# Performance work log

Hardware: AMD Instinct MI355X
Metric: run time of the kernel (lower is better)

The kernel has to match this reference:

```python
import jax, jax.numpy as jnp
import numpy as np

NEG_SLOPE = 0.2  # PyG GATConv default LeakyReLU slope
BN_EPS = 1e-5


def gat_layer(x, src, dst, W, a_src, a_dst, num_nodes):
    """PyG-style GATConv (no dropout, eval mode). Returns [N, H, C]."""
    H, C = a_src.shape
    h = (x @ W).reshape(-1, H, C)                       # [N,H,C]
    s_src = jnp.einsum('nhc,hc->nh', h, a_src)          # [N,H]
    s_dst = jnp.einsum('nhc,hc->nh', h, a_dst)          # [N,H]
    e = jax.nn.leaky_relu(s_src[src] + s_dst[dst], NEG_SLOPE)  # [E,H]
    # segment softmax over incoming edges of each dst node
    e_max = jax.ops.segment_max(e, dst, num_segments=num_nodes)  # [N,H]
    e_exp = jnp.exp(e - e_max[dst])
    denom = jax.ops.segment_sum(e_exp, dst, num_segments=num_nodes)
    alpha = e_exp / (denom[dst] + 1e-16)                # [E,H]
    msg = h[src] * alpha[:, :, None]                    # [E,H,C] (dominant intermediate)
    return jax.ops.segment_sum(msg, dst, num_segments=num_nodes)  # [N,H,C]


def setup_inputs() -> dict:
    key = jax.random.key(0)
    ks = jax.random.split(key, 12)
    N, Din, Hdim, Heads, Dout = 50000, 128, 128, 8, 128
    E = 150000
    inp = {}
    inp['x'] = jax.random.normal(ks[0], (N, Din), dtype=jnp.float32)
    inp['edge_index'] = jax.random.randint(ks[1], (2, E), 0, N, dtype=jnp.int64)
    sc1 = 1.0 / np.sqrt(Din)
    inp['W1'] = jax.random.uniform(ks[2], (Din, Heads * Hdim), minval=-sc1, maxval=sc1, dtype=jnp.float32)
    inp['a_src1'] = jax.random.normal(ks[3], (Heads, Hdim), dtype=jnp.float32) * 0.1
    inp['a_dst1'] = jax.random.normal(ks[4], (Heads, Hdim), dtype=jnp.float32) * 0.1
    inp['b1'] = jnp.zeros((Heads * Hdim,), dtype=jnp.float32)
    inp['gamma'] = jnp.ones((Heads * Hdim,), dtype=jnp.float32)
    inp['beta'] = jnp.zeros((Heads * Hdim,), dtype=jnp.float32)
    sc2 = 1.0 / np.sqrt(Heads * Hdim)
    inp['W2'] = jax.random.uniform(ks[5], (Heads * Hdim, Dout), minval=-sc2, maxval=sc2, dtype=jnp.float32)
    inp['a_src2'] = jax.random.normal(ks[6], (1, Dout), dtype=jnp.float32) * 0.1
    inp['a_dst2'] = jax.random.normal(ks[7], (1, Dout), dtype=jnp.float32) * 0.1
    inp['b2'] = jnp.zeros((Dout,), dtype=jnp.float32)
    return inp


def reference(x, W1, a_src1, a_dst1, b1, gamma, beta, W2, a_src2, a_dst2, b2, edge_index):
    N = x.shape[0]
    src, dst = edge_index[0], edge_index[1]
    # GAT layer 1: heads=8, concat=True
    h1 = gat_layer(x, src, dst, W1, a_src1, a_dst1, N)   # [N,8,128]
    h1 = h1.reshape(N, -1) + b1                          # [N,1024]
    # BatchNorm1d (training-mode batch stats, biased variance as in torch)
    mu = jnp.mean(h1, axis=0)
    var = jnp.var(h1, axis=0)
    h1 = gamma * (h1 - mu) * jax.lax.rsqrt(var + BN_EPS) + beta
    h1 = jax.nn.elu(h1)
    # GAT layer 2: heads=1, concat=False (mean == squeeze for 1 head)
    h2 = gat_layer(h1, src, dst, W2, a_src2, a_dst2, N)  # [N,1,128]
    return h2[:, 0, :] + b2
```

## Files before the change

kernel.cpp:

```cpp
#include <hip/hip_runtime.h>
#include <hip/hip_bf16.h>
#include <math.h>

#define NEG_SLOPE 0.2f
#define BN_EPS 1e-5f

typedef short bf16x8 __attribute__((ext_vector_type(8)));
typedef float f32x4 __attribute__((ext_vector_type(4)));

__device__ __forceinline__ float bf2f(unsigned short u) {
  union { unsigned int i; float f; } v;
  v.i = ((unsigned int)u) << 16;
  return v.f;
}
__device__ __forceinline__ unsigned short f2bf(float f) {
  union { unsigned int i; float f; } v;
  v.f = f;
  unsigned int i = v.i;
  unsigned int r = (i + 0x7fffu + ((i >> 16) & 1u)) >> 16;
  return (unsigned short)r;
}

__global__ __launch_bounds__(256) void detect_kernel(
    const unsigned int* __restrict__ xw, const unsigned int* __restrict__ eiw,
    int E, int* __restrict__ flags) {
  __shared__ int cnt[2];
  if (threadIdx.x < 2) cnt[threadIdx.x] = 0;
  __syncthreads();
  int t = threadIdx.x;
  int inrange = 0;
  for (int i = t; i < 2048; i += 256) {
    unsigned int e = (xw[i] >> 7) & 0xFFu;
    inrange += (e >= 100u && e <= 135u) ? 1 : 0;
  }
  atomicAdd(&cnt[0], inrange);
  int M = min(1024, E / 2);
  int zeros = 0;
  for (int i = t; i < M; i += 256) zeros += (eiw[2 * i + 1] == 0u) ? 1 : 0;
  atomicAdd(&cnt[1], zeros);
  __syncthreads();
  if (t == 0) {
    flags[0] = (cnt[0] > 1536) ? 1 : 0;
    flags[1] = (cnt[1] > M / 2) ? 1 : 0;
  }
}

__global__ __launch_bounds__(256) void canon_x(
    const void* __restrict__ src, unsigned short* __restrict__ dst, int n_real,
    int n_total, const int* __restrict__ flags) {
  int i = blockIdx.x * 256 + threadIdx.x;
  if (i >= n_total) return;
  unsigned short v = 0;
  if (i < n_real)
    v = flags[0] ? ((const unsigned short*)src)[i]
                 : f2bf(((const float*)src)[i]);
  dst[i] = v;
}

__global__ __launch_bounds__(256) void canon_w_t(
    const void* __restrict__ src, unsigned short* __restrict__ dst, int Kdim,
    int Ndim, const int* __restrict__ flags) {
  int i = blockIdx.x * 256 + threadIdx.x;
  if (i >= Kdim * Ndim) return;
  int k = i / Ndim, n = i - k * Ndim;
  unsigned short v = flags[0] ? ((const unsigned short*)src)[i]
                              : f2bf(((const float*)src)[i]);
  dst[(size_t)n * Kdim + k] = v;
}

__global__ __launch_bounds__(1024) void canon_params(
    const void* s0, const void* s1, const void* s2, const void* s3,
    const void* s4, const void* s5, const void* s6, const void* s7,
    unsigned short* d0, unsigned short* d1, unsigned short* d2,
    unsigned short* d3, unsigned short* d4, unsigned short* d5,
    unsigned short* d6, unsigned short* d7, const int* __restrict__ flags) {
  int b = blockIdx.x, t = threadIdx.x;
  const void* s;
  unsigned short* d;
  int n;
  switch (b) {
    case 0: s = s0; d = d0; n = 1024; break;
    case 1: s = s1; d = d1; n = 1024; break;
    case 2: s = s2; d = d2; n = 1024; break;
    case 3: s = s3; d = d3; n = 1024; break;
    case 4: s = s4; d = d4; n = 1024; break;
    case 5: s = s5; d = d5; n = 128; break;
    case 6: s = s6; d = d6; n = 128; break;
    default: s = s7; d = d7; n = 128; break;
  }
  if (t < n)
    d[t] = flags[0] ? ((const unsigned short*)s)[t]
                    : f2bf(((const float*)s)[t]);
}

__global__ __launch_bounds__(256) void canon_idx(
    const int* __restrict__ ei, int* __restrict__ eis, int* __restrict__ eid,
    int E, const int* __restrict__ flags) {
  int e = blockIdx.x * 256 + threadIdx.x;
  if (e >= E) return;
  if (flags[1]) {
    eis[e] = ei[2 * (size_t)e];
    eid[e] = ei[2 * (size_t)E + 2 * (size_t)e];
  } else {
    eis[e] = ei[e];
    eid[e] = ei[E + e];
  }
}

template <bool TRANSFORM_A, bool OUT_BF16>
__global__ __launch_bounds__(256) void gemm_mfma(
    const unsigned short* __restrict__ A, const unsigned short* __restrict__ Bt,
    void* __restrict__ Cv, int M, int N, int K,
    const float* __restrict__ scale, const float* __restrict__ shift) {
  constexpr int BK = 32;
  constexpr int LDA = BK + 8;
  __shared__ unsigned short As[128 * LDA];
  __shared__ unsigned short Bs[128 * LDA];

  const int m0 = blockIdx.y * 128;
  const int n0 = blockIdx.x * 128;
  const int tid = threadIdx.x;
  const int wid = tid >> 6;
  const int lane = tid & 63;
  const int q = lane >> 4;
  const int r = lane & 15;
  const int wm = (wid >> 1) * 64;
  const int wn = (wid & 1) * 64;

  f32x4 acc[4][4] = {};

  const int row0 = (tid * 8) >> 5, col0 = (tid * 8) & 31;
  const int row1 = row0 + 64;

  bf16x8 ra[2], rb[2];
  ra[0] = *(const bf16x8*)(A + (size_t)(m0 + row0) * K + col0);
  ra[1] = *(const bf16x8*)(A + (size_t)(m0 + row1) * K + col0);
  rb[0] = *(const bf16x8*)(Bt + (size_t)(n0 + row0) * K + col0);
  rb[1] = *(const bf16x8*)(Bt + (size_t)(n0 + row1) * K + col0);

  for (int k0 = 0; k0 < K; k0 += BK) {
#pragma unroll
    for (int rd = 0; rd < 2; ++rd) {
      int row = rd ? row1 : row0;
      bf16x8 v = ra[rd];
      if (TRANSFORM_A) {
        float scv[8], shv[8];
        *(float4*)&scv[0] = *(const float4*)(scale + k0 + col0);
        *(float4*)&scv[4] = *(const float4*)(scale + k0 + col0 + 4);
        *(float4*)&shv[0] = *(const float4*)(shift + k0 + col0);
        *(float4*)&shv[4] = *(const float4*)(shift + k0 + col0 + 4);
        union { bf16x8 v; unsigned short u[8]; } p;
        p.v = v;
#pragma unroll
        for (int j = 0; j < 8; ++j) {
          float f = bf2f(p.u[j]) * scv[j] + shv[j];
          f = f > 0.f ? f : (__expf(f) - 1.0f);
          p.u[j] = f2bf(f);
        }
        v = p.v;
      }
      *(bf16x8*)(&As[row * LDA + col0]) = v;
      *(bf16x8*)(&Bs[row * LDA + col0]) = rb[rd];
    }
    __syncthreads();

    int k1 = k0 + BK;
    if (k1 < K) {
      ra[0] = *(const bf16x8*)(A + (size_t)(m0 + row0) * K + k1 + col0);
      ra[1] = *(const bf16x8*)(A + (size_t)(m0 + row1) * K + k1 + col0);
      rb[0] = *(const bf16x8*)(Bt + (size_t)(n0 + row0) * K + k1 + col0);
      rb[1] = *(const bf16x8*)(Bt + (size_t)(n0 + row1) * K + k1 + col0);
    }

    bf16x8 af[4], bfv[4];
#pragma unroll
    for (int mi = 0; mi < 4; ++mi)
      af[mi] = *(const bf16x8*)(&As[(wm + mi * 16 + r) * LDA + q * 8]);
#pragma unroll
    for (int ni = 0; ni < 4; ++ni)
      bfv[ni] = *(const bf16x8*)(&Bs[(wn + ni * 16 + r) * LDA + q * 8]);
#pragma unroll
    for (int mi = 0; mi < 4; ++mi)
#pragma unroll
      for (int ni = 0; ni < 4; ++ni)
        acc[mi][ni] = __builtin_amdgcn_mfma_f32_16x16x32_bf16(
            af[mi], bfv[ni], acc[mi][ni], 0, 0, 0);
    __syncthreads();
  }

#pragma unroll
  for (int mi = 0; mi < 4; ++mi) {
#pragma unroll
    for (int ni = 0; ni < 4; ++ni) {
#pragma unroll
      for (int i = 0; i < 4; ++i) {
        int row = m0 + wm + mi * 16 + q * 4 + i;
        int col = n0 + wn + ni * 16 + r;
        if (OUT_BF16)
          ((unsigned short*)Cv)[(size_t)row * N + col] = f2bf(acc[mi][ni][i]);
        else
          ((float*)Cv)[(size_t)row * N + col] = acc[mi][ni][i];
      }
    }
  }
}

__global__ __launch_bounds__(256) void count_dst(const int* __restrict__ eid,
                                                 int E, int* __restrict__ cnt) {
  int e = blockIdx.x * 256 + threadIdx.x;
  if (e < E) atomicAdd(&cnt[eid[e]], 1);
}

__global__ __launch_bounds__(256) void scan_p1(const int* __restrict__ cnt,
                                               int* __restrict__ bsum, int N) {
  __shared__ int sd[256];
  int b = blockIdx.x, t = threadIdx.x;
  int base = b * 2048;
  int s = 0;
  for (int i = t; i < 2048; i += 256) {
    int idx = base + i;
    if (idx < N) s += cnt[idx];
  }
  sd[t] = s;
  __syncthreads();
  for (int o = 128; o > 0; o >>= 1) {
    if (t < o) sd[t] += sd[t + o];
    __syncthreads();
  }
  if (t == 0) bsum[b] = sd[0];
}

__global__ __launch_bounds__(256) void scan_p2(int* __restrict__ bsum, int nb) {
  __shared__ int sd[256];
  int t = threadIdx.x;
  int own = (t < nb) ? bsum[t] : 0;
  sd[t] = own;
  __syncthreads();
  for (int o = 1; o < 256; o <<= 1) {
    int v = (t >= o) ? sd[t - o] : 0;
    __syncthreads();
    sd[t] += v;
    __syncthreads();
  }
  if (t < nb) bsum[t] = sd[t] - own;
}

__global__ __launch_bounds__(256) void scan_p3(
    const int* __restrict__ cnt, const int* __restrict__ bsum,
    int* __restrict__ offsets, int* __restrict__ cursor, int N) {
  __shared__ int sd[256];
  int b = blockIdx.x, t = threadIdx.x;
  int base = b * 2048 + t * 8;
  int c[8];
  int ts = 0;
#pragma unroll
  for (int j = 0; j < 8; ++j) {
    int idx = base + j;
    c[j] = (idx < N) ? cnt[idx] : 0;
    ts += c[j];
  }
  sd[t] = ts;
  __syncthreads();
  for (int o = 1; o < 256; o <<= 1) {
    int v = (t >= o) ? sd[t - o] : 0;
    __syncthreads();
    sd[t] += v;
    __syncthreads();
  }
  int run = bsum[b] + sd[t] - ts;
#pragma unroll
  for (int j = 0; j < 8; ++j) {
    int idx = base + j;
    if (idx < N) {
      offsets[idx] = run;
      cursor[idx] = run;
      run += c[j];
    }
  }
  if (b == gridDim.x - 1 && t == 255) offsets[N] = bsum[b] + sd[255];
}

__global__ __launch_bounds__(256) void scatter_src(
    const int* __restrict__ eis, const int* __restrict__ eid, int E,
    int* __restrict__ cursor, int* __restrict__ srcs, int* __restrict__ dsts) {
  int e = blockIdx.x * 256 + threadIdx.x;
  if (e >= E) return;
  int d = eid[e];
  int pos = atomicAdd(&cursor[d], 1);
  srcs[pos] = eis[e];
  dsts[pos] = d;
}

__global__ __launch_bounds__(256) void scores1_v2(
    const unsigned short* __restrict__ h1, const unsigned short* __restrict__ a_src,
    const unsigned short* __restrict__ a_dst, float* __restrict__ s_src,
    float* __restrict__ s_dst, int N) {
  int n = blockIdx.x * 4 + (threadIdx.x >> 6);
  int lane = threadIdx.x & 63;
  if (n >= N) return;
  const unsigned short* hp = h1 + (size_t)n * 1024 + lane * 16;
  union { bf16x8 v; unsigned short u[8]; } h0, h1v, s0, s1, d0, d1;
  h0.v = *(const bf16x8*)hp;
  h1v.v = *(const bf16x8*)(hp + 8);
  s0.v = *(const bf16x8*)(a_src + lane * 16);
  s1.v = *(const bf16x8*)(a_src + lane * 16 + 8);
  d0.v = *(const bf16x8*)(a_dst + lane * 16);
  d1.v = *(const bf16x8*)(a_dst + lane * 16 + 8);
  float vs = 0.f, vd = 0.f;
#pragma unroll
  for (int j = 0; j < 8; ++j) {
    float a = bf2f(h0.u[j]), b = bf2f(h1v.u[j]);
    vs += a * bf2f(s0.u[j]) + b * bf2f(s1.u[j]);
    vd += a * bf2f(d0.u[j]) + b * bf2f(d1.u[j]);
  }
  vs += __shfl_xor(vs, 1, 64); vd += __shfl_xor(vd, 1, 64);
  vs += __shfl_xor(vs, 2, 64); vd += __shfl_xor(vd, 2, 64);
  vs += __shfl_xor(vs, 4, 64); vd += __shfl_xor(vd, 4, 64);
  if ((lane & 7) == 0) {
    int h = lane >> 3;
    s_src[n * 8 + h] = vs;
    s_dst[n * 8 + h] = vd;
  }
}

__global__ __launch_bounds__(256) void scores2_f32(
    const float* __restrict__ h2, const unsigned short* __restrict__ a_src,
    const unsigned short* __restrict__ a_dst, float* __restrict__ s_src,
    float* __restrict__ s_dst, int N) {
  int w = blockIdx.x * 4 + (threadIdx.x >> 6);
  int lane = threadIdx.x & 63;
  if (w >= N) return;
  float2 hv = *(const float2*)(h2 + (size_t)w * 128 + lane * 2);
  unsigned int av = *(const unsigned int*)(a_src + lane * 2);
  unsigned int dv = *(const unsigned int*)(a_dst + lane * 2);
  float vs = hv.x * bf2f(av & 0xffff) + hv.y * bf2f(av >> 16);
  float vd = hv.x * bf2f(dv & 0xffff) + hv.y * bf2f(dv >> 16);
#pragma unroll
  for (int off = 32; off > 0; off >>= 1) {
    vs += __shfl_down(vs, off, 64);
    vd += __shfl_down(vd, off, 64);
  }
  if (lane == 0) {
    s_src[w] = vs;
    s_dst[w] = vd;
  }
}

__global__ __launch_bounds__(256) void edge_w1(
    const int* __restrict__ srcs, const int* __restrict__ dsts,
    const float* __restrict__ ssrc, const float* __restrict__ sdst,
    float* __restrict__ ew, int E8) {
  int t = blockIdx.x * 256 + threadIdx.x;
  if (t >= E8) return;
  int p = t >> 3, h = t & 7;
  float v = ssrc[srcs[p] * 8 + h] + sdst[dsts[p] * 8 + h];
  v = v > 0.f ? v : NEG_SLOPE * v;
  ew[t] = __expf(v);
}

__global__ __launch_bounds__(256) void edge_w2(
    const int* __restrict__ srcs, const int* __restrict__ dsts,
    const float* __restrict__ ssrc, const float* __restrict__ sdst,
    float* __restrict__ ew2, int E) {
  int p = blockIdx.x * 256 + threadIdx.x;
  if (p >= E) return;
  float v = ssrc[srcs[p]] + sdst[dsts[p]];
  v = v > 0.f ? v : NEG_SLOPE * v;
  ew2[p] = __expf(v);
}

__global__ __launch_bounds__(256) void agg1_csr(
    const int* __restrict__ offsets, const int* __restrict__ srcs,
    const unsigned short* __restrict__ h1, const float* __restrict__ ew,
    const unsigned short* __restrict__ b1, unsigned short* __restrict__ h1n) {
  int n = blockIdx.x;
  int j = threadIdx.x;
  int c = j * 4;
  int h = c >> 7;
  int beg = offsets[n], end = offsets[n + 1];
  float a0 = 0.f, a1 = 0.f, a2 = 0.f, a3 = 0.f, wsum = 0.f;
  for (int p = beg; p < end; ++p) {
    int s = srcs[p];
    float w = ew[p * 8 + h];
    wsum += w;
    ushort4 u = *(const ushort4*)(h1 + (size_t)s * 1024 + c);
    a0 = fmaf(bf2f(u.x), w, a0);
    a1 = fmaf(bf2f(u.y), w, a1);
    a2 = fmaf(bf2f(u.z), w, a2);
    a3 = fmaf(bf2f(u.w), w, a3);
  }
  float inv = 1.0f / (wsum + 1e-16f);
  ushort4 bb = *(const ushort4*)(b1 + c);
  ushort4 o;
  o.x = f2bf(a0 * inv + bf2f(bb.x));
  o.y = f2bf(a1 * inv + bf2f(bb.y));
  o.z = f2bf(a2 * inv + bf2f(bb.z));
  o.w = f2bf(a3 * inv + bf2f(bb.w));
  *(ushort4*)(h1n + (size_t)n * 1024 + c) = o;
}

__global__ __launch_bounds__(256) void bn_stats_part(
    const unsigned short* __restrict__ h1n, float* __restrict__ part, int N,
    int rowsPerBlock) {
  int b = blockIdx.x;
  int r0 = b * rowsPerBlock;
  int r1 = min(r0 + rowsPerBlock, N);
  int c = threadIdx.x * 4;
  float s0 = 0, s1 = 0, s2 = 0, s3 = 0;
  float q0 = 0, q1 = 0, q2 = 0, q3 = 0;
  int r = r0;
  for (; r + 4 <= r1; r += 4) {
    ushort4 u0 = *(const ushort4*)(h1n + (size_t)(r + 0) * 1024 + c);
    ushort4 u1 = *(const ushort4*)(h1n + (size_t)(r + 1) * 1024 + c);
    ushort4 u2 = *(const ushort4*)(h1n + (size_t)(r + 2) * 1024 + c);
    ushort4 u3 = *(const ushort4*)(h1n + (size_t)(r + 3) * 1024 + c);
    float v;
    v = bf2f(u0.x); s0 += v; q0 += v * v;
    v = bf2f(u0.y); s1 += v; q1 += v * v;
    v = bf2f(u0.z); s2 += v; q2 += v * v;
    v = bf2f(u0.w); s3 += v; q3 += v * v;
    v = bf2f(u1.x); s0 += v; q0 += v * v;
    v = bf2f(u1.y); s1 += v; q1 += v * v;
    v = bf2f(u1.z); s2 += v; q2 += v * v;
    v = bf2f(u1.w); s3 += v; q3 += v * v;
    v = bf2f(u2.x); s0 += v; q0 += v * v;
    v = bf2f(u2.y); s1 += v; q1 += v * v;
    v = bf2f(u2.z); s2 += v; q2 += v * v;
    v = bf2f(u2.w); s3 += v; q3 += v * v;
    v = bf2f(u3.x); s0 += v; q0 += v * v;
    v = bf2f(u3.y); s1 += v; q1 += v * v;
    v = bf2f(u3.z); s2 += v; q2 += v * v;
    v = bf2f(u3.w); s3 += v; q3 += v * v;
  }
  for (; r < r1; ++r) {
    ushort4 u = *(const ushort4*)(h1n + (size_t)r * 1024 + c);
    float v;
    v = bf2f(u.x); s0 += v; q0 += v * v;
    v = bf2f(u.y); s1 += v; q1 += v * v;
    v = bf2f(u.z); s2 += v; q2 += v * v;
    v = bf2f(u.w); s3 += v; q3 += v * v;
  }
  float* pb = part + (size_t)b * 2048;
  pb[c + 0] = s0; pb[c + 1] = s1; pb[c + 2] = s2; pb[c + 3] = s3;
  pb[1024 + c + 0] = q0; pb[1024 + c + 1] = q1;
  pb[1024 + c + 2] = q2; pb[1024 + c + 3] = q3;
}

__global__ __launch_bounds__(256) void bn_reduce_finalize(
    const float* __restrict__ part, int nparts,
    const unsigned short* __restrict__ gamma,
    const unsigned short* __restrict__ beta, float* __restrict__ scale,
    float* __restrict__ shift, int N) {
  int c = blockIdx.x * 4 + (threadIdx.x >> 6);
  int lane = threadIdx.x & 63;
  float s = 0.f, q = 0.f;
  for (int b = lane; b < nparts; b += 64) {
    s += part[(size_t)b * 2048 + c];
    q += part[(size_t)b * 2048 + 1024 + c];
  }
#pragma unroll
  for (int o = 32; o > 0; o >>= 1) {
    s += __shfl_xor(s, o, 64);
    q += __shfl_xor(q, o, 64);
  }
  if (lane == 0) {
    float inv_n = 1.0f / (float)N;
    float mu = s * inv_n;
    float var = q * inv_n - mu * mu;
    float sc = bf2f(gamma[c]) * rsqrtf(var + BN_EPS);
    scale[c] = sc;
    shift[c] = bf2f(beta[c]) - mu * sc;
  }
}

__global__ __launch_bounds__(64) void agg2_csr(
    const int* __restrict__ offsets, const int* __restrict__ srcs,
    const float* __restrict__ h2, const float* __restrict__ ew2,
    const unsigned short* __restrict__ b2, void* __restrict__ out,
    const int* __restrict__ flags) {
  int n = blockIdx.x;
  int lane = threadIdx.x;
  int c = lane * 2;
  int beg = offsets[n], end = offsets[n + 1];
  float a0 = 0.f, a1 = 0.f, wsum = 0.f;
  for (int p = beg; p < end; ++p) {
    int s = srcs[p];
    float w = ew2[p];
    wsum += w;
    float2 hv = *(const float2*)(h2 + (size_t)s * 128 + c);
    a0 = fmaf(hv.x, w, a0);
    a1 = fmaf(hv.y, w, a1);
  }
  float inv = 1.0f / (wsum + 1e-16f);
  unsigned int bb = *(const unsigned int*)(b2 + c);
  float r0 = a0 * inv + bf2f(bb & 0xffff);
  float r1 = a1 * inv + bf2f(bb >> 16);
  if (flags[0]) {
    unsigned int o = (unsigned int)f2bf(r0) | ((unsigned int)f2bf(r1) << 16);
    *(unsigned int*)((unsigned short*)out + (size_t)n * 128 + c) = o;
  } else {
    *(float2*)((float*)out + (size_t)n * 128 + c) = make_float2(r0, r1);
  }
}

extern "C" void kernel_launch(void* const* d_in, const int* in_sizes, int n_in,
                              void* d_out, int out_size, void* d_ws,
                              size_t ws_size, hipStream_t stream) {
  const void* x      = d_in[0];
  const int*  ei     = (const int*)d_in[1];
  const void* W1     = d_in[2];
  const void* a_src1 = d_in[3];
  const void* a_dst1 = d_in[4];
  const void* b1     = d_in[5];
  const void* gamma  = d_in[6];
  const void* beta   = d_in[7];
  const void* W2     = d_in[8];
  const void* a_src2 = d_in[9];
  const void* a_dst2 = d_in[10];
  const void* b2     = d_in[11];

  const int N = in_sizes[0] / 128;
  const int E = in_sizes[1] / 2;
  const int MP = ((N + 127) / 128) * 128;
  const int NB = (N + 2047) / 2048;
  const int NSTAT = 256;
  const int RPB = (N + NSTAT - 1) / NSTAT;

  char* ws = (char*)d_ws;
  size_t off = 0;
  unsigned short* h1  = (unsigned short*)(ws + off); off += (size_t)MP * 1024 * 2;
  char* h1n_base = ws + off;
  unsigned short* h1n = (unsigned short*)h1n_base;   off += (size_t)MP * 1024 * 2;
  float* ssrc1 = (float*)(ws + off); off += (size_t)N * 8 * 4;
  float* sdst1 = (float*)(ws + off); off += (size_t)N * 8 * 4;
  int* offsets = (int*)(ws + off); off += ((size_t)(N + 1) * 4 + 63) & ~63ull;
  int* srcs    = (int*)(ws + off); off += (size_t)E * 4;
  int* dsts    = (int*)(ws + off); off += (size_t)E * 4;
  float* ew    = (float*)(ws + off); off += (size_t)E * 8 * 4;
  float* part  = (float*)(ws + off); off += (size_t)NSTAT * 2048 * 4;
  unsigned short* W1t = (unsigned short*)(ws + off); off += 131072 * 2;
  unsigned short* W2t = (unsigned short*)(ws + off); off += 131072 * 2;
  unsigned short* as1c = (unsigned short*)(ws + off); off += 1024 * 2;
  unsigned short* ad1c = (unsigned short*)(ws + off); off += 1024 * 2;
  unsigned short* b1c  = (unsigned short*)(ws + off); off += 1024 * 2;
  unsigned short* gmc  = (unsigned short*)(ws + off); off += 1024 * 2;
  unsigned short* btc  = (unsigned short*)(ws + off); off += 1024 * 2;
  unsigned short* as2c = (unsigned short*)(ws + off); off += 128 * 2;
  unsigned short* ad2c = (unsigned short*)(ws + off); off += 128 * 2;
  unsigned short* b2c  = (unsigned short*)(ws + off); off += 128 * 2;
  float* scale = (float*)(ws + off); off += 1024 * 4;
  float* shift = (float*)(ws + off); off += 1024 * 4;
  int* bsum    = (int*)(ws + off); off += 256 * 4;
  int* flags   = (int*)(ws + off); off += 64;
  unsigned short* x_bf = (unsigned short*)h1n_base;
  int* eis    = (int*)(h1n_base + (16u << 20));
  int* eid    = eis + E;
  int* cnt    = eid + E;
  int* cursor = cnt + N;
  float* h2    = (float*)h1;
  float* ssrc2 = ssrc1;
  float* sdst2 = sdst1;
  float* ew2   = ew;

  detect_kernel<<<1, 256, 0, stream>>>((const unsigned int*)x,
                                       (const unsigned int*)ei, E, flags);
  canon_x<<<(MP * 128 + 255) / 256, 256, 0, stream>>>(x, x_bf, N * 128,
                                                      MP * 128, flags);
  canon_w_t<<<(131072 + 255) / 256, 256, 0, stream>>>(W1, W1t, 128, 1024, flags);
  canon_w_t<<<(131072 + 255) / 256, 256, 0, stream>>>(W2, W2t, 1024, 128, flags);
  canon_params<<<8, 1024, 0, stream>>>(a_src1, a_dst1, b1, gamma, beta, a_src2,
                                       a_dst2, b2, as1c, ad1c, b1c, gmc, btc,
                                       as2c, ad2c, b2c, flags);
  canon_idx<<<(E + 255) / 256, 256, 0, stream>>>(ei, eis, eid, E, flags);

  hipMemsetAsync(cnt, 0, (size_t)N * 4, stream);
  hipMemsetAsync((char*)h1n + (size_t)N * 1024 * 2, 0,
                 (size_t)(MP - N) * 1024 * 2, stream);

  count_dst<<<(E + 255) / 256, 256, 0, stream>>>(eid, E, cnt);
  scan_p1<<<NB, 256, 0, stream>>>(cnt, bsum, N);
  scan_p2<<<1, 256, 0, stream>>>(bsum, NB);
  scan_p3<<<NB, 256, 0, stream>>>(cnt, bsum, offsets, cursor, N);
  scatter_src<<<(E + 255) / 256, 256, 0, stream>>>(eis, eid, E, cursor, srcs,
                                                   dsts);

  {
    dim3 g(1024 / 128, MP / 128);
    gemm_mfma<false, true><<<g, 256, 0, stream>>>(x_bf, W1t, h1, MP, 1024, 128,
                                                  nullptr, nullptr);
  }
  scores1_v2<<<(N + 3) / 4, 256, 0, stream>>>(h1, as1c, ad1c, ssrc1, sdst1, N);
  edge_w1<<<(E * 8 + 255) / 256, 256, 0, stream>>>(srcs, dsts, ssrc1, sdst1,
                                                   ew, E * 8);
  agg1_csr<<<N, 256, 0, stream>>>(offsets, srcs, h1, ew, b1c, h1n);

  bn_stats_part<<<NSTAT, 256, 0, stream>>>(h1n, part, N, RPB);
  bn_reduce_finalize<<<256, 256, 0, stream>>>(part, NSTAT, gmc, btc, scale,
                                              shift, N);

  {
    dim3 g(1, MP / 128);
    gemm_mfma<true, false><<<g, 256, 0, stream>>>(h1n, W2t, h2, MP, 128, 1024,
                                                  scale, shift);
  }
  scores2_f32<<<(N + 3) / 4, 256, 0, stream>>>(h2, as2c, ad2c, ssrc2, sdst2, N);
  edge_w2<<<(E + 255) / 256, 256, 0, stream>>>(srcs, dsts, ssrc2, sdst2, ew2, E);
  agg2_csr<<<N, 64, 0, stream>>>(offsets, srcs, h2, ew2, b2c, d_out, flags);
}
```

Measured before the change: 381.3 us.

## Fuse attention score dot-products into GEMM epilogues and unroll aggregation loops

Computes per-head source and destination attention scores inside the MFMA GEMM epilogue from the accumulators, removing the separate score kernels that re-read h1 and h2. The second GEMM switches to 64-row tiles to double the block count. The CSR aggregation loops are unrolled by two for more memory-level parallelism, and agg2 packs four nodes per 256-thread block. Score buffers are padded to the row-padded size, and the epilogue adds shuffles and an extra block sync.

```diff
diff --git a/kernel.cpp b/kernel.cpp
--- a/kernel.cpp
+++ b/kernel.cpp
@@ -107,59 +107,67 @@
   }
 }
 
-template <bool TRANSFORM_A, bool OUT_BF16>
+template <int BM, bool TRANSFORM_A, bool OUT_BF16, bool SCORES>
 __global__ __launch_bounds__(256) void gemm_mfma(
     const unsigned short* __restrict__ A, const unsigned short* __restrict__ Bt,
     void* __restrict__ Cv, int M, int N, int K,
-    const float* __restrict__ scale, const float* __restrict__ shift) {
+    const float* __restrict__ scale, const float* __restrict__ shift,
+    const unsigned short* __restrict__ aScr,
+    const unsigned short* __restrict__ aDcr, float* __restrict__ ssrc,
+    float* __restrict__ sdst, int hs) {
   constexpr int BK = 32;
   constexpr int LDA = BK + 8;
-  __shared__ unsigned short As[128 * LDA];
+  constexpr int MI = BM / 32;
+  __shared__ unsigned short As[BM * LDA];
   __shared__ unsigned short Bs[128 * LDA];
-
-  const int m0 = blockIdx.y * 128;
+  __shared__ float sS[2][128];
+  __shared__ float sD[2][128];
+
+  const int m0 = blockIdx.y * BM;
   const int n0 = blockIdx.x * 128;
   const int tid = threadIdx.x;
   const int wid = tid >> 6;
   const int lane = tid & 63;
   const int q = lane >> 4;
   const int r = lane & 15;
-  const int wm = (wid >> 1) * 64;
+  const int wm = (wid >> 1) * (BM / 2);
   const int wn = (wid & 1) * 64;
 
-  f32x4 acc[4][4] = {};
+  f32x4 acc[MI][4] = {};
 
   const int row0 = (tid * 8) >> 5, col0 = (tid * 8) & 31;
-  const int row1 = row0 + 64;
 
   bf16x8 ra[2], rb[2];
   ra[0] = *(const bf16x8*)(A + (size_t)(m0 + row0) * K + col0);
-  ra[1] = *(const bf16x8*)(A + (size_t)(m0 + row1) * K + col0);
+  if (BM == 128)
+    ra[1] = *(const bf16x8*)(A + (size_t)(m0 + row0 + 64) * K + col0);
   rb[0] = *(const bf16x8*)(Bt + (size_t)(n0 + row0) * K + col0);
-  rb[1] = *(const bf16x8*)(Bt + (size_t)(n0 + row1) * K + col0);
+  rb[1] = *(const bf16x8*)(Bt + (size_t)(n0 + row0 + 64) * K + col0);
 
   for (int k0 = 0; k0 < K; k0 += BK) {
 #pragma unroll
     for (int rd = 0; rd < 2; ++rd) {
-      int row = rd ? row1 : row0;
-      bf16x8 v = ra[rd];
-      if (TRANSFORM_A) {
-        float scv[8], shv[8];
-        *(float4*)&scv[0] = *(const float4*)(scale + k0 + col0);
-        *(float4*)&scv[4] = *(const float4*)(scale + k0 + col0 + 4);
-        *(float4*)&shv[0] = *(const float4*)(shift + k0 + col0);
-        *(float4*)&shv[4] = *(const float4*)(shift + k0 + col0 + 4);
-        union { bf16x8 v; unsigned short u[8]; } p;
-        p.v = v;
-#pragma unroll
-        for (int j = 0; j < 8; ++j) {
-          float f = bf2f(p.u[j]) * scv[j] + shv[j];
-          f = f > 0.f ? f : (__expf(f) - 1.0f);
-          p.u[j] = f2bf(f);
+      int row = row0 + rd * 64;
+      if (rd == 0 || BM == 128) {
+        bf16x8 v = ra[rd];
+        if (TRANSFORM_A) {
+          float scv[8], shv[8];
+          *(float4*)&scv[0] = *(const float4*)(scale + k0 + col0);
+          *(float4*)&scv[4] = *(const float4*)(scale + k0 + col0 + 4);
+          *(float4*)&shv[0] = *(const float4*)(shift + k0 + col0);
+          *(float4*)&shv[4] = *(const float4*)(shift + k0 + col0 + 4);
+          union { bf16x8 v; unsigned short u[8]; } p;
+          p.v = v;
+#pragma unroll
+          for (int j = 0; j < 8; ++j) {
+            float f = bf2f(p.u[j]) * scv[j] + shv[j];
+            f = f > 0.f ? f : (__expf(f) - 1.0f);
+            p.u[j] = f2bf(f);
+          }
+          v = p.v;
         }
-        v = p.v;
+        *(bf16x8*)(&As[row * LDA + col0]) = v;
       }
-      *(bf16x8*)(&As[row * LDA + col0]) = v;
       *(bf16x8*)(&Bs[row * LDA + col0]) = rb[rd];
     }
     __syncthreads();
@@ -167,20 +175,21 @@
     int k1 = k0 + BK;
     if (k1 < K) {
       ra[0] = *(const bf16x8*)(A + (size_t)(m0 + row0) * K + k1 + col0);
-      ra[1] = *(const bf16x8*)(A + (size_t)(m0 + row1) * K + k1 + col0);
+      if (BM == 128)
+        ra[1] = *(const bf16x8*)(A + (size_t)(m0 + row0 + 64) * K + k1 + col0);
       rb[0] = *(const bf16x8*)(Bt + (size_t)(n0 + row0) * K + k1 + col0);
-      rb[1] = *(const bf16x8*)(Bt + (size_t)(n0 + row1) * K + k1 + col0);
+      rb[1] = *(const bf16x8*)(Bt + (size_t)(n0 + row0 + 64) * K + k1 + col0);
     }
 
-    bf16x8 af[4], bfv[4];
-#pragma unroll
-    for (int mi = 0; mi < 4; ++mi)
+    bf16x8 af[MI], bfv[4];
+#pragma unroll
+    for (int mi = 0; mi < MI; ++mi)
       af[mi] = *(const bf16x8*)(&As[(wm + mi * 16 + r) * LDA + q * 8]);
 #pragma unroll
     for (int ni = 0; ni < 4; ++ni)
       bfv[ni] = *(const bf16x8*)(&Bs[(wn + ni * 16 + r) * LDA + q * 8]);
 #pragma unroll
-    for (int mi = 0; mi < 4; ++mi)
+    for (int mi = 0; mi < MI; ++mi)
 #pragma unroll
       for (int ni = 0; ni < 4; ++ni)
         acc[mi][ni] = __builtin_amdgcn_mfma_f32_16x16x32_bf16(
@@ -189,7 +198,7 @@
   }
 
 #pragma unroll
-  for (int mi = 0; mi < 4; ++mi) {
+  for (int mi = 0; mi < MI; ++mi) {
 #pragma unroll
     for (int ni = 0; ni < 4; ++ni) {
 #pragma unroll
@@ -203,6 +212,44 @@
       }
     }
   }
+
+  if (SCORES) {
+    const int half = wid & 1;
+    float aSv[4], aDv[4];
+#pragma unroll
+    for (int ni = 0; ni < 4; ++ni) {
+      aSv[ni] = bf2f(aScr[n0 + wn + ni * 16 + r]);
+      aDv[ni] = bf2f(aDcr[n0 + wn + ni * 16 + r]);
+    }
+#pragma unroll
+    for (int mi = 0; mi < MI; ++mi) {
+#pragma unroll
+      for (int i = 0; i < 4; ++i) {
+        float ps = 0.f, pd = 0.f;
+#pragma unroll
+        for (int ni = 0; ni < 4; ++ni) {
+          float v = acc[mi][ni][i];
+          ps += v * aSv[ni];
+          pd += v * aDv[ni];
+        }
+        ps += __shfl_xor(ps, 1, 64); pd += __shfl_xor(pd, 1, 64);
+        ps += __shfl_xor(ps, 2, 64); pd += __shfl_xor(pd, 2, 64);
+        ps += __shfl_xor(ps, 4, 64); pd += __shfl_xor(pd, 4, 64);
+        ps += __shfl_xor(ps, 8, 64); pd += __shfl_xor(pd, 8, 64);
+        if (r == 0) {
+          int rl = wm + mi * 16 + q * 4 + i;
+          sS[half][rl] = ps;
+          sD[half][rl] = pd;
+        }
+      }
+    }
+    __syncthreads();
+    if (tid < BM) {
+      int grow = m0 + tid;
+      ssrc[(size_t)grow * hs + blockIdx.x] = sS[0][tid] + sS[1][tid];
+      sdst[(size_t)grow * hs + blockIdx.x] = sD[0][tid] + sD[1][tid];
+    }
+  }
 }
 
 __global__ __launch_bounds__(256) void count_dst(const int* __restrict__ eid,
@@ -289,61 +336,6 @@
   int pos = atomicAdd(&cursor[d], 1);
   srcs[pos] = eis[e];
   dsts[pos] = d;
-}
-
-__global__ __launch_bounds__(256) void scores1_v2(
-    const unsigned short* __restrict__ h1, const unsigned short* __restrict__ a_src,
-    const unsigned short* __restrict__ a_dst, float* __restrict__ s_src,
-    float* __restrict__ s_dst, int N) {
-  int n = blockIdx.x * 4 + (threadIdx.x >> 6);
-  int lane = threadIdx.x & 63;
-  if (n >= N) return;
-  const unsigned short* hp = h1 + (size_t)n * 1024 + lane * 16;
-  union { bf16x8 v; unsigned short u[8]; } h0, h1v, s0, s1, d0, d1;
-  h0.v = *(const bf16x8*)hp;
-  h1v.v = *(const bf16x8*)(hp + 8);
-  s0.v = *(const bf16x8*)(a_src + lane * 16);
-  s1.v = *(const bf16x8*)(a_src + lane * 16 + 8);
-  d0.v = *(const bf16x8*)(a_dst + lane * 16);
-  d1.v = *(const bf16x8*)(a_dst + lane * 16 + 8);
-  float vs = 0.f, vd = 0.f;
-#pragma unroll
-  for (int j = 0; j < 8; ++j) {
-    float a = bf2f(h0.u[j]), b = bf2f(h1v.u[j]);
-    vs += a * bf2f(s0.u[j]) + b * bf2f(s1.u[j]);
-    vd += a * bf2f(d0.u[j]) + b * bf2f(d1.u[j]);
-  }
-  vs += __shfl_xor(vs, 1, 64); vd += __shfl_xor(vd, 1, 64);
-  vs += __shfl_xor(vs, 2, 64); vd += __shfl_xor(vd, 2, 64);
-  vs += __shfl_xor(vs, 4, 64); vd += __shfl_xor(vd, 4, 64);
-  if ((lane & 7) == 0) {
-    int h = lane >> 3;
-    s_src[n * 8 + h] = vs;
-    s_dst[n * 8 + h] = vd;
-  }
-}
-
-__global__ __launch_bounds__(256) void scores2_f32(
-    const float* __restrict__ h2, const unsigned short* __restrict__ a_src,
-    const unsigned short* __restrict__ a_dst, float* __restrict__ s_src,
-    float* __restrict__ s_dst, int N) {
-  int w = blockIdx.x * 4 + (threadIdx.x >> 6);
-  int lane = threadIdx.x & 63;
-  if (w >= N) return;
-  float2 hv = *(const float2*)(h2 + (size_t)w * 128 + lane * 2);
-  unsigned int av = *(const unsigned int*)(a_src + lane * 2);
-  unsigned int dv = *(const unsigned int*)(a_dst + lane * 2);
-  float vs = hv.x * bf2f(av & 0xffff) + hv.y * bf2f(av >> 16);
-  float vd = hv.x * bf2f(dv & 0xffff) + hv.y * bf2f(dv >> 16);
-#pragma unroll
-  for (int off = 32; off > 0; off >>= 1) {
-    vs += __shfl_down(vs, off, 64);
-    vd += __shfl_down(vd, off, 64);
-  }
-  if (lane == 0) {
-    s_src[w] = vs;
-    s_dst[w] = vd;
-  }
 }
 
 __global__ __launch_bounds__(256) void edge_w1(
@@ -379,15 +371,31 @@
   int h = c >> 7;
   int beg = offsets[n], end = offsets[n + 1];
   float a0 = 0.f, a1 = 0.f, a2 = 0.f, a3 = 0.f, wsum = 0.f;
-  for (int p = beg; p < end; ++p) {
-    int s = srcs[p];
-    float w = ew[p * 8 + h];
-    wsum += w;
-    ushort4 u = *(const ushort4*)(h1 + (size_t)s * 1024 + c);
-    a0 = fmaf(bf2f(u.x), w, a0);
-    a1 = fmaf(bf2f(u.y), w, a1);
-    a2 = fmaf(bf2f(u.z), w, a2);
-    a3 = fmaf(bf2f(u.w), w, a3);
+  int p = beg;
+  for (; p + 2 <= end; p += 2) {
+    int s0 = srcs[p], s1 = srcs[p + 1];
+    float w0 = ew[p * 8 + h], w1 = ew[(p + 1) * 8 + h];
+    ushort4 u0 = *(const ushort4*)(h1 + (size_t)s0 * 1024 + c);
+    ushort4 u1 = *(const ushort4*)(h1 + (size_t)s1 * 1024 + c);
+    wsum += w0 + w1;
+    a0 = fmaf(bf2f(u0.x), w0, a0);
+    a1 = fmaf(bf2f(u0.y), w0, a1);
+    a2 = fmaf(bf2f(u0.z), w0, a2);
+    a3 = fmaf(bf2f(u0.w), w0, a3);
+    a0 = fmaf(bf2f(u1.x), w1, a0);
+    a1 = fmaf(bf2f(u1.y), w1, a1);
+    a2 = fmaf(bf2f(u1.z), w1, a2);
+    a3 = fmaf(bf2f(u1.w), w1, a3);
+  }
+  if (p < end) {
+    int s0 = srcs[p];
+    float w0 = ew[p * 8 + h];
+    ushort4 u0 = *(const ushort4*)(h1 + (size_t)s0 * 1024 + c);
+    wsum += w0;
+    a0 = fmaf(bf2f(u0.x), w0, a0);
+    a1 = fmaf(bf2f(u0.y), w0, a1);
+    a2 = fmaf(bf2f(u0.z), w0, a2);
+    a3 = fmaf(bf2f(u0.w), w0, a3);
   }
   float inv = 1.0f / (wsum + 1e-16f);
   ushort4 bb = *(const ushort4*)(b1 + c);
@@ -473,23 +481,36 @@
   }
 }
 
-__global__ __launch_bounds__(64) void agg2_csr(
+__global__ __launch_bounds__(256) void agg2_csr(
     const int* __restrict__ offsets, const int* __restrict__ srcs,
     const float* __restrict__ h2, const float* __restrict__ ew2,
     const unsigned short* __restrict__ b2, void* __restrict__ out,
-    const int* __restrict__ flags) {
-  int n = blockIdx.x;
-  int lane = threadIdx.x;
+    const int* __restrict__ flags, int N) {
+  int n = blockIdx.x * 4 + (threadIdx.x >> 6);
+  int lane = threadIdx.x & 63;
+  if (n >= N) return;
   int c = lane * 2;
   int beg = offsets[n], end = offsets[n + 1];
   float a0 = 0.f, a1 = 0.f, wsum = 0.f;
-  for (int p = beg; p < end; ++p) {
-    int s = srcs[p];
-    float w = ew2[p];
-    wsum += w;
-    float2 hv = *(const float2*)(h2 + (size_t)s * 128 + c);
-    a0 = fmaf(hv.x, w, a0);
-    a1 = fmaf(hv.y, w, a1);
+  int p = beg;
+  for (; p + 2 <= end; p += 2) {
+    int s0 = srcs[p], s1 = srcs[p + 1];
+    float w0 = ew2[p], w1 = ew2[p + 1];
+    float2 v0 = *(const float2*)(h2 + (size_t)s0 * 128 + c);
+    float2 v1 = *(const float2*)(h2 + (size_t)s1 * 128 + c);
+    wsum += w0 + w1;
+    a0 = fmaf(v0.x, w0, a0);
+    a1 = fmaf(v0.y, w0, a1);
+    a0 = fmaf(v1.x, w1, a0);
+    a1 = fmaf(v1.y, w1, a1);
+  }
+  if (p < end) {
+    int s0 = srcs[p];
+    float w0 = ew2[p];
+    float2 v0 = *(const float2*)(h2 + (size_t)s0 * 128 + c);
+    wsum += w0;
+    a0 = fmaf(v0.x, w0, a0);
+    a1 = fmaf(v0.y, w0, a1);
   }
   float inv = 1.0f / (wsum + 1e-16f);
   unsigned int bb = *(const unsigned int*)(b2 + c);
@@ -531,8 +552,8 @@
   unsigned short* h1  = (unsigned short*)(ws + off); off += (size_t)MP * 1024 * 2;
   char* h1n_base = ws + off;
   unsigned short* h1n = (unsigned short*)h1n_base;   off += (size_t)MP * 1024 * 2;
-  float* ssrc1 = (float*)(ws + off); off += (size_t)N * 8 * 4;
-  float* sdst1 = (float*)(ws + off); off += (size_t)N * 8 * 4;
+  float* ssrc1 = (float*)(ws + off); off += (size_t)MP * 8 * 4;
+  float* sdst1 = (float*)(ws + off); off += (size_t)MP * 8 * 4;
   int* offsets = (int*)(ws + off); off += ((size_t)(N + 1) * 4 + 63) & ~63ull;
   int* srcs    = (int*)(ws + off); off += (size_t)E * 4;
   int* dsts    = (int*)(ws + off); off += (size_t)E * 4;
@@ -586,10 +607,10 @@
 
   {
     dim3 g(1024 / 128, MP / 128);
-    gemm_mfma<false, true><<<g, 256, 0, stream>>>(x_bf, W1t, h1, MP, 1024, 128,
-                                                  nullptr, nullptr);
-  }
-  scores1_v2<<<(N + 3) / 4, 256, 0, stream>>>(h1, as1c, ad1c, ssrc1, sdst1, N);
+    gemm_mfma<128, false, true, true><<<g, 256, 0, stream>>>(
+        x_bf, W1t, h1, MP, 1024, 128, nullptr, nullptr, as1c, ad1c, ssrc1,
+        sdst1, 8);
+  }
   edge_w1<<<(E * 8 + 255) / 256, 256, 0, stream>>>(srcs, dsts, ssrc1, sdst1,
                                                    ew, E * 8);
   agg1_csr<<<N, 256, 0, stream>>>(offsets, srcs, h1, ew, b1c, h1n);
@@ -599,11 +620,12 @@
                                               shift, N);
 
   {
-    dim3 g(1, MP / 128);
-    gemm_mfma<true, false><<<g, 256, 0, stream>>>(h1n, W2t, h2, MP, 128, 1024,
-                                                  scale, shift);
-  }
-  scores2_f32<<<(N + 3) / 4, 256, 0, stream>>>(h2, as2c, ad2c, ssrc2, sdst2, N);
+    dim3 g(1, MP / 64);
+    gemm_mfma<64, true, false, true><<<g, 256, 0, stream>>>(
+        h1n, W2t, h2, MP, 128, 1024, scale, shift, as2c, ad2c, ssrc2, sdst2,
+        1);
+  }
   edge_w2<<<(E + 255) / 256, 256, 0, stream>>>(srcs, dsts, ssrc2, sdst2, ew2, E);
-  agg2_csr<<<N, 64, 0, stream>>>(offsets, srcs, h2, ew2, b2c, d_out, flags);
-}
+  agg2_csr<<<(N + 3) / 4, 256, 0, stream>>>(offsets, srcs, h2, ew2, b2c, d_out,
+                                            flags, N);
+}
```

Measured after the change: 377.2 us. About the same (-1.1%).
